# Kernel tuning notes

Hardware: AMD Instinct MI355X
Metric: run time of the kernel (lower is better)

Reference implementation:

```python
import jax, jax.numpy as jnp
import numpy as np

N, IN, OUT, T = 32768, 512, 512, 8


def setup_inputs() -> dict:
    key = jax.random.key(0)
    k1, k2, k3 = jax.random.split(key, 3)
    x = jax.random.normal(k1, (N, IN), dtype=jnp.float32)
    x_type = jax.random.randint(k2, (N,), 0, T, dtype=jnp.int32)
    # xavier_uniform with relu gain, per torch reset_parameters
    gain = np.sqrt(2.0)
    bound = gain * np.sqrt(6.0 / (IN + OUT))
    W = jax.random.uniform(k3, (T, IN, OUT), dtype=jnp.float32,
                           minval=-bound, maxval=bound)
    return {"x": x, "x_type": x_type, "W": W}


def reference(x, x_type, W):
    # gather_mm semantics: out[i] = x[i] @ W[x_type[i]]
    # Expressed as a small fixed loop over types (T=8) with masking, which
    # avoids materializing the [N, IN, OUT] gathered weight tensor.
    num_types = W.shape[0]
    out = jnp.zeros((x.shape[0], W.shape[2]), dtype=x.dtype)
    for t in range(num_types):
        mask = (x_type == t)[:, None]  # [N, 1]
        out = out + jnp.where(mask, x @ W[t], jnp.zeros((), dtype=x.dtype))
    return out
```

## Files before the change

kernel.cpp:

```cpp
#include <hip/hip_runtime.h>
#include <hip/hip_bf16.h>

#define N_ROWS 32768
#define K_DIM 512
#define OUT_DIM 512
#define N_TYPES 8
#define BM 64
#define BN 256
#define BK 64
#define TPB 512

typedef __attribute__((ext_vector_type(8))) short bf16x8;
typedef __attribute__((ext_vector_type(4))) float f32x4;

__device__ inline ushort f2bf(float f) {
    __hip_bfloat16 h = __float2bfloat16(f);
    return *reinterpret_cast<ushort*>(&h);
}

__device__ inline void gload_lds16(const void* g, void* l) {
    __builtin_amdgcn_global_load_lds(
        (const __attribute__((address_space(1))) void*)g,
        (__attribute__((address_space(3))) void*)l, 16, 0, 0);
}

__global__ void k_fill(const int* __restrict__ x_type, int* meta, int* __restrict__ row_ids) {
    __shared__ int lcnt[N_TYPES];
    __shared__ int lbase[N_TYPES];
    if (threadIdx.x < N_TYPES) lcnt[threadIdx.x] = 0;
    __syncthreads();
    int i = blockIdx.x * 256 + threadIdx.x;
    int t = x_type[i];
    int lpos = atomicAdd(&lcnt[t], 1);
    __syncthreads();
    if (threadIdx.x < N_TYPES)
        lbase[threadIdx.x] = (lcnt[threadIdx.x] > 0)
            ? atomicAdd(&meta[threadIdx.x], lcnt[threadIdx.x]) : 0;
    __syncthreads();
    row_ids[(size_t)t * N_ROWS + lbase[t] + lpos] = i;
}

__global__ void k_wt(const float* __restrict__ W, ushort* __restrict__ Wt) {
    __shared__ float tile[64][65];
    int t = blockIdx.x, kb = blockIdx.y, cb = blockIdx.z;
    const float* src = W + (size_t)t * K_DIM * OUT_DIM + (size_t)kb * 64 * OUT_DIM + cb * 64;
    #pragma unroll
    for (int j = 0; j < 16; ++j) {
        int idx = threadIdx.x + j * 256;
        int r = idx >> 6, c = idx & 63;
        tile[r][c] = src[(size_t)r * OUT_DIM + c];
    }
    __syncthreads();
    ushort* dst = Wt + (size_t)t * OUT_DIM * K_DIM + (size_t)(cb * 64) * K_DIM + kb * 64;
    #pragma unroll
    for (int j = 0; j < 16; ++j) {
        int idx = threadIdx.x + j * 256;
        int cc = idx >> 6, kk = idx & 63;
        dst[(size_t)cc * K_DIM + kk] = f2bf(tile[kk][cc]);
    }
}

__global__ __launch_bounds__(512, 4) void k_gemm13(
    const float* __restrict__ x, const ushort* __restrict__ Wt,
    const int* __restrict__ meta, const int* __restrict__ row_ids,
    float* __restrict__ out) {

    __shared__ ushort As[BM * BK];
    __shared__ ushort Bs[BN * BK];
    __shared__ int rids[BM];

    int b = blockIdx.x;
    int type = b >> 9;
    int r0 = (b & (TPB - 1)) * BM;
    if (r0 >= meta[type]) return;

    int tid = threadIdx.x;
    int wave = tid >> 6, lane = tid & 63;

    if (tid < BM) rids[tid] = row_ids[(size_t)type * N_ROWS + r0 + tid];
    __syncthreads();

    int c0 = blockIdx.y * BN;
    const ushort* Wtt = Wt + (size_t)type * OUT_DIM * K_DIM + (size_t)c0 * K_DIM;

    int sa_row  = tid >> 3;
    int sa_slot = tid & 7;
    int sa_rid  = rids[sa_row];
    const float* sa_src = x + (size_t)max(sa_rid, 0) * K_DIM + sa_slot * 8;
    int sa_byte = (sa_row * 128 + sa_slot * 16) ^ ((sa_row & 7) << 4);

    int sb_colgrp = lane >> 3;
    int sb_koff   = (((lane & 7) * 16) ^ (sb_colgrp << 4)) >> 1;

    int wrb = (wave >> 2) * 32;
    int wcb = (wave & 3) * 64;
    int lrow = lane & 15;
    int lkb16 = (lane >> 4) * 16;

    f32x4 acc[2][4] = {};

    #pragma unroll 1
    for (int kk = 0; kk < K_DIM; kk += BK) {
        #pragma unroll
        for (int j = 0; j < 4; ++j) {
            int chunk = wave * 4 + j;
            int col = chunk * 8 + sb_colgrp;
            gload_lds16(Wtt + (size_t)col * K_DIM + kk + sb_koff,
                        (char*)Bs + chunk * 1024);
        }
        {
            ushort tmp[8] = {0, 0, 0, 0, 0, 0, 0, 0};
            if (sa_rid >= 0) {
                float4 v0 = *reinterpret_cast<const float4*>(sa_src + kk);
                float4 v1 = *reinterpret_cast<const float4*>(sa_src + kk + 4);
                tmp[0] = f2bf(v0.x); tmp[1] = f2bf(v0.y); tmp[2] = f2bf(v0.z); tmp[3] = f2bf(v0.w);
                tmp[4] = f2bf(v1.x); tmp[5] = f2bf(v1.y); tmp[6] = f2bf(v1.z); tmp[7] = f2bf(v1.w);
            }
            *reinterpret_cast<uint4*>((char*)As + sa_byte) = *reinterpret_cast<const uint4*>(tmp);
        }
        __syncthreads();

        #pragma unroll
        for (int s = 0; s < 2; ++s) {
            bf16x8 af[2], bfr[4];
            #pragma unroll
            for (int mi = 0; mi < 2; ++mi) {
                int row = wrb + mi * 16 + lrow;
                int byte = (row * 128 + s * 64 + lkb16) ^ ((row & 7) << 4);
                af[mi] = *reinterpret_cast<const bf16x8*>((const char*)As + byte);
            }
            #pragma unroll
            for (int ni = 0; ni < 4; ++ni) {
                int col = wcb + ni * 16 + lrow;
                int byte = (col * 128 + s * 64 + lkb16) ^ ((col & 7) << 4);
                bfr[ni] = *reinterpret_cast<const bf16x8*>((const char*)Bs + byte);
            }
            #pragma unroll
            for (int mi = 0; mi < 2; ++mi)
                #pragma unroll
                for (int ni = 0; ni < 4; ++ni)
                    acc[mi][ni] = __builtin_amdgcn_mfma_f32_16x16x32_bf16(
                        af[mi], bfr[ni], acc[mi][ni], 0, 0, 0);
        }
        __syncthreads();
    }

    int rgrp = (lane >> 4) * 4;
    #pragma unroll
    for (int mi = 0; mi < 2; ++mi) {
        #pragma unroll
        for (int rr = 0; rr < 4; ++rr) {
            int lr = wrb + mi * 16 + rgrp + rr;
            int gr = rids[lr];
            if (gr >= 0) {
                float* dst = out + (size_t)gr * OUT_DIM + c0 + wcb;
                #pragma unroll
                for (int ni = 0; ni < 4; ++ni)
                    dst[ni * 16 + lrow] = acc[mi][ni][rr];
            }
        }
    }
}

extern "C" void kernel_launch(void* const* d_in, const int* in_sizes, int n_in,
                              void* d_out, int out_size, void* d_ws, size_t ws_size,
                              hipStream_t stream) {
    const float* x      = (const float*)d_in[0];
    const int*   x_type = (const int*)d_in[1];
    const float* W      = (const float*)d_in[2];
    float* out          = (float*)d_out;

    char* ws = (char*)d_ws;
    size_t off_rids = 256;
    size_t off_wt   = off_rids + sizeof(int) * (size_t)N_TYPES * N_ROWS;
    int* meta    = (int*)ws;
    int* row_ids = (int*)(ws + off_rids);
    ushort* Wt   = (ushort*)(ws + off_wt);

    hipMemsetAsync(meta, 0, sizeof(int) * N_TYPES, stream);
    hipMemsetAsync(row_ids, 0xFF, sizeof(int) * (size_t)N_TYPES * N_ROWS, stream);
    k_fill<<<N_ROWS / 256, 256, 0, stream>>>(x_type, meta, row_ids);

    dim3 wgrid(N_TYPES, K_DIM / 64, OUT_DIM / 64);
    k_wt<<<wgrid, 256, 0, stream>>>(W, Wt);

    dim3 ggrid(N_TYPES * TPB, OUT_DIM / BN);
    k_gemm13<<<ggrid, 512, 0, stream>>>(x, Wt, meta, row_ids, out);
}
```

Before: 62.12 us.

## Double-buffer LDS tiles with BK=32 to overlap loads with MFMA

Switches the grouped GEMM main loop to a double-buffered scheme. The next K-slice of W goes straight to LDS and the next x slice goes into registers while the current slice is multiplied, which removes one barrier per iteration. BK is halved to 32 so both buffers fit in the same LDS footprint, and the swizzle layouts change to match. In exchange there are twice as many iterations and barriers, smaller loads per step, and the x prefetch keeps more registers live.

```diff
diff --git a/kernel.cpp b/kernel.cpp
--- a/kernel.cpp
+++ b/kernel.cpp
@@ -7,8 +7,11 @@
 #define N_TYPES 8
 #define BM 64
 #define BN 256
-#define BK 64
+#define BK 32
+#define NT (K_DIM / BK)
 #define TPB 512
+#define ABUF 4096
+#define BBUF 16384
 
 typedef __attribute__((ext_vector_type(8))) short bf16x8;
 typedef __attribute__((ext_vector_type(4))) float f32x4;
@@ -60,13 +63,13 @@
     }
 }
 
-__global__ __launch_bounds__(512, 4) void k_gemm13(
+__global__ __launch_bounds__(512, 4) void k_gemm15(
     const float* __restrict__ x, const ushort* __restrict__ Wt,
     const int* __restrict__ meta, const int* __restrict__ row_ids,
     float* __restrict__ out) {
 
-    __shared__ ushort As[BM * BK];
-    __shared__ ushort Bs[BN * BK];
+    __shared__ ushort As[2 * BM * BK];
+    __shared__ ushort Bs[2 * BN * BK];
     __shared__ int rids[BM];
 
     int b = blockIdx.x;
@@ -86,66 +89,87 @@
     int sa_row  = tid >> 3;
     int sa_slot = tid & 7;
     int sa_rid  = rids[sa_row];
-    const float* sa_src = x + (size_t)max(sa_rid, 0) * K_DIM + sa_slot * 8;
-    int sa_byte = (sa_row * 128 + sa_slot * 16) ^ ((sa_row & 7) << 4);
-
-    int sb_colgrp = lane >> 3;
-    int sb_koff   = (((lane & 7) * 16) ^ (sb_colgrp << 4)) >> 1;
+    const float* sa_src = x + (size_t)max(sa_rid, 0) * K_DIM + sa_slot * 4;
+    int sa_byte = sa_row * 64 + (((sa_slot >> 1) ^ (sa_row & 3)) * 16) + (sa_slot & 1) * 8;
+
+    int sb_col  = lane >> 2;
+    int sb_srcg = (lane & 3) ^ (sb_col & 3);
 
     int wrb = (wave >> 2) * 32;
     int wcb = (wave & 3) * 64;
     int lrow = lane & 15;
-    int lkb16 = (lane >> 4) * 16;
+    int g4   = lane >> 4;
 
     f32x4 acc[2][4] = {};
 
-    #pragma unroll 1
-    for (int kk = 0; kk < K_DIM; kk += BK) {
-        #pragma unroll
-        for (int j = 0; j < 4; ++j) {
-            int chunk = wave * 4 + j;
-            int col = chunk * 8 + sb_colgrp;
-            gload_lds16(Wtt + (size_t)col * K_DIM + kk + sb_koff,
-                        (char*)Bs + chunk * 1024);
+#define STAGE_B(buf, t)                                                         \
+    _Pragma("unroll")                                                           \
+    for (int j = 0; j < 2; ++j) {                                               \
+        int chunk = wave * 2 + j;                                               \
+        int col = chunk * 16 + sb_col;                                          \
+        gload_lds16(Wtt + (size_t)col * K_DIM + (t) * BK + sb_srcg * 8,         \
+                    (char*)Bs + (buf) * BBUF + chunk * 1024);                   \
+    }
+
+#define LOAD_X(t, v)                                                            \
+    v = (sa_rid >= 0)                                                           \
+        ? *reinterpret_cast<const float4*>(sa_src + (t) * BK)                   \
+        : float4{0.f, 0.f, 0.f, 0.f};
+
+#define WRITE_A(buf, v)                                                         \
+    {                                                                           \
+        ushort tmp[4] = { f2bf(v.x), f2bf(v.y), f2bf(v.z), f2bf(v.w) };         \
+        *reinterpret_cast<uint2*>((char*)As + (buf) * ABUF + sa_byte) =         \
+            *reinterpret_cast<const uint2*>(tmp);                               \
+    }
+
+#define COMPUTE(buf)                                                            \
+    {                                                                           \
+        bf16x8 af[2], bfr[4];                                                   \
+        _Pragma("unroll")                                                       \
+        for (int mi = 0; mi < 2; ++mi) {                                        \
+            int row = wrb + mi * 16 + lrow;                                     \
+            int byte = (buf) * ABUF + row * 64 + ((g4 ^ (row & 3)) * 16);       \
+            af[mi] = *reinterpret_cast<const bf16x8*>((const char*)As + byte);  \
+        }                                                                       \
+        _Pragma("unroll")                                                       \
+        for (int ni = 0; ni < 4; ++ni) {                                        \
+            int col = wcb + ni * 16 + lrow;                                     \
+            int byte = (buf) * BBUF + col * 64 + ((g4 ^ (col & 3)) * 16);       \
+            bfr[ni] = *reinterpret_cast<const bf16x8*>((const char*)Bs + byte); \
+        }                                                                       \
+        _Pragma("unroll")                                                       \
+        for (int mi = 0; mi < 2; ++mi)                                          \
+            _Pragma("unroll")                                                   \
+            for (int ni = 0; ni < 4; ++ni)                                      \
+                acc[mi][ni] = __builtin_amdgcn_mfma_f32_16x16x32_bf16(          \
+                    af[mi], bfr[ni], acc[mi][ni], 0, 0, 0);                     \
+    }
+
+    STAGE_B(0, 0)
+    {
+        float4 v;
+        LOAD_X(0, v)
+        WRITE_A(0, v)
+    }
+    __syncthreads();
+
+    #pragma unroll 2
+    for (int t = 0; t < NT; ++t) {
+        int cur = t & 1;
+        float4 v;
+        if (t < NT - 1) {
+            STAGE_B(cur ^ 1, t + 1)
+            LOAD_X(t + 1, v)
         }
-        {
-            ushort tmp[8] = {0, 0, 0, 0, 0, 0, 0, 0};
-            if (sa_rid >= 0) {
-                float4 v0 = *reinterpret_cast<const float4*>(sa_src + kk);
-                float4 v1 = *reinterpret_cast<const float4*>(sa_src + kk + 4);
-                tmp[0] = f2bf(v0.x); tmp[1] = f2bf(v0.y); tmp[2] = f2bf(v0.z); tmp[3] = f2bf(v0.w);
-                tmp[4] = f2bf(v1.x); tmp[5] = f2bf(v1.y); tmp[6] = f2bf(v1.z); tmp[7] = f2bf(v1.w);
-            }
-            *reinterpret_cast<uint4*>((char*)As + sa_byte) = *reinterpret_cast<const uint4*>(tmp);
+        COMPUTE(cur)
+        if (t < NT - 1) {
+            WRITE_A(cur ^ 1, v)
+            __syncthreads();
         }
-        __syncthreads();
-
-        #pragma unroll
-        for (int s = 0; s < 2; ++s) {
-            bf16x8 af[2], bfr[4];
-            #pragma unroll
-            for (int mi = 0; mi < 2; ++mi) {
-                int row = wrb + mi * 16 + lrow;
-                int byte = (row * 128 + s * 64 + lkb16) ^ ((row & 7) << 4);
-                af[mi] = *reinterpret_cast<const bf16x8*>((const char*)As + byte);
-            }
-            #pragma unroll
-            for (int ni = 0; ni < 4; ++ni) {
-                int col = wcb + ni * 16 + lrow;
-                int byte = (col * 128 + s * 64 + lkb16) ^ ((col & 7) << 4);
-                bfr[ni] = *reinterpret_cast<const bf16x8*>((const char*)Bs + byte);
-            }
-            #pragma unroll
-            for (int mi = 0; mi < 2; ++mi)
-                #pragma unroll
-                for (int ni = 0; ni < 4; ++ni)
-                    acc[mi][ni] = __builtin_amdgcn_mfma_f32_16x16x32_bf16(
-                        af[mi], bfr[ni], acc[mi][ni], 0, 0, 0);
-        }
-        __syncthreads();
-    }
-
-    int rgrp = (lane >> 4) * 4;
+    }
+
+    int rgrp = g4 * 4;
     #pragma unroll
     for (int mi = 0; mi < 2; ++mi) {
         #pragma unroll
@@ -185,5 +209,5 @@
     k_wt<<<wgrid, 256, 0, stream>>>(W, Wt);
 
     dim3 ggrid(N_TYPES * TPB, OUT_DIM / BN);
-    k_gemm13<<<ggrid, 512, 0, stream>>>(x, Wt, meta, row_ids, out);
-}
+    k_gemm15<<<ggrid, 512, 0, stream>>>(x, Wt, meta, row_ids, out);
+}
```

Measured after the change: 68.94 us. +11.0%, slower.
